# Kernel tuning notes

Hardware: AMD Instinct MI355X
Metric: run time of the kernel (lower is better)

Reference implementation:

```python
import jax, jax.numpy as jnp
import numpy as np
import math

B, S, H, NH = 2, 2048, 1024, 16
DH = H // NH  # head_dim = 64


def setup_inputs() -> dict:
    key = jax.random.key(0)
    k1, k2, k3 = jax.random.split(key, 3)
    hidden_states = jax.random.normal(k1, (B, S, H), dtype=jnp.float32)
    # causal additive mask: 0 on/below diagonal, large negative above
    causal = jnp.tril(jnp.ones((S, S), dtype=jnp.float32))
    attention_mask = jnp.where(causal == 1, 0.0, -1e9).astype(jnp.float32)
    attention_mask = jnp.broadcast_to(attention_mask[None, None], (B, 1, S, S))
    w_qkv = jax.random.normal(k2, (H, 3 * H), dtype=jnp.float32) * (H ** -0.5)
    w_out = jax.random.normal(k3, (H, H), dtype=jnp.float32) * (H ** -0.5)
    return {"hidden_states": hidden_states, "attention_mask": attention_mask,
            "w_qkv": w_qkv, "w_out": w_out}


def reference(hidden_states, attention_mask, w_qkv, w_out):
    # fused QKV projection (bias-free Linear)
    qkv = hidden_states @ w_qkv                       # [B,S,3H]
    qkv = qkv.reshape(B, S, 3, NH, DH)
    qkv = jnp.transpose(qkv, (2, 0, 3, 1, 4))         # [3,B,NH,S,DH]
    q, k, v = qkv[0], qkv[1], qkv[2]
    scores = jnp.einsum('bhqd,bhkd->bhqk', q, k) / math.sqrt(DH)
    scores = scores + attention_mask                  # [B,NH,S,S]
    probs = jax.nn.softmax(scores, axis=-1)
    ctx = jnp.einsum('bhqk,bhkd->bhqd', probs, v)     # [B,NH,S,DH]
    ctx = jnp.transpose(ctx, (0, 2, 1, 3)).reshape(B, S, H)
    return ctx @ w_out                                # [B,S,H]
```

## Files before the change

### kernel.cpp

```cpp
#include <hip/hip_runtime.h>

#define S_LEN 2048
#define NHEAD 16
#define DHEAD 64
#define HDIM  1024
#define BATCH 2
#define MTOK  (BATCH * S_LEN)

using bf16x8 = __bf16 __attribute__((ext_vector_type(8)));
using f32x4  = float __attribute__((ext_vector_type(4)));
using f32x16 = float __attribute__((ext_vector_type(16)));
using u16x4  = unsigned short __attribute__((ext_vector_type(4)));
using u32x4a = unsigned __attribute__((ext_vector_type(4)));

typedef unsigned short ushort_t;

static __device__ __forceinline__ ushort_t f2bf(float f) {
  union { float f; unsigned u; } v{f};
  unsigned r = v.u + 0x7FFFu + ((v.u >> 16) & 1u);
  return (ushort_t)(r >> 16);
}

static __device__ __forceinline__ unsigned pkbf(float a, float b) {
  return ((unsigned)f2bf(b) << 16) | (unsigned)f2bf(a);
}

static __device__ __forceinline__ unsigned cvtpk(float a, float b) {
  unsigned r;
  asm("v_cvt_pk_bf16_f32 %0, %1, %2" : "=v"(r) : "v"(a), "v"(b));
  return r;
}

static __device__ __forceinline__ bf16x8 mk8(unsigned a, unsigned b, unsigned c, unsigned d) {
  u32x4a t = {a, b, c, d};
  return __builtin_bit_cast(bf16x8, t);
}

static __device__ __forceinline__ void gload_lds16(const void* g, void* lds) {
  __builtin_amdgcn_global_load_lds(
      (const __attribute__((address_space(1))) void*)g,
      (__attribute__((address_space(3))) void*)lds, 16, 0, 0);
}

static __device__ __forceinline__ float bpermf(int paddr, float v) {
  return __builtin_bit_cast(float,
      __builtin_amdgcn_ds_bpermute(paddr, __builtin_bit_cast(int, v)));
}
static __device__ __forceinline__ unsigned bpermu(int paddr, unsigned v) {
  return (unsigned)__builtin_amdgcn_ds_bpermute(paddr, (int)v);
}

__global__ __launch_bounds__(256) void cast_bf16(const float* __restrict__ in,
                                                 ushort_t* __restrict__ out, int n4) {
  int i = blockIdx.x * blockDim.x + threadIdx.x;
  if (i >= n4) return;
  float4 v = *((const float4*)in + i);
  u16x4 o = { f2bf(v.x), f2bf(v.y), f2bf(v.z), f2bf(v.w) };
  *((u16x4*)out + i) = o;
}

__global__ void transpose_cast(const float* __restrict__ in, ushort_t* __restrict__ out,
                               int R, int C) {
  __shared__ float tile[32][33];
  int bx = blockIdx.x, by = blockIdx.y;
  int tx = threadIdx.x, ty = threadIdx.y;
  #pragma unroll
  for (int i = 0; i < 32; i += 8)
    tile[ty + i][tx] = in[(size_t)(by * 32 + ty + i) * C + bx * 32 + tx];
  __syncthreads();
  #pragma unroll
  for (int i = 0; i < 32; i += 8)
    out[(size_t)(bx * 32 + ty + i) * R + by * 32 + tx] = f2bf(tile[tx][ty + i]);
}

__global__ __launch_bounds__(512, 4) void gemm_2ph(
    const ushort_t* __restrict__ A, const ushort_t* __restrict__ Bt,
    int M, int N, int K, int mode,
    ushort_t* __restrict__ outQ, ushort_t* __restrict__ outK, ushort_t* __restrict__ outV,
    float* __restrict__ outF) {
  __shared__ __align__(16) ushort_t lA[2][128 * 32];
  __shared__ __align__(16) ushort_t lB[2][128 * 32];
  const int wg = blockIdx.x;
  const int nst = (int)(gridDim.x >> 7);
  const int xcd = wg & 7;
  const int idx = wg >> 3;
  const int stg = xcd * nst + (idx >> 4);
  const int sbm = idx & 3, sbn = (idx >> 2) & 3;
  const int bm = (stg & 7) * 4 + sbm;
  const int bn = (stg >> 3) * 4 + sbn;
  const int tid = threadIdx.x;
  const int wv = tid >> 6, lane = tid & 63;
  const int wm = wv >> 2, wn = wv & 3;
  const int lo = lane & 15, hi = lane >> 4;

  f32x4 acc[4][2] = {};

  const int srow = tid >> 2;
  const int schunk = (tid & 3) ^ ((tid >> 3) & 3);
  const ushort_t* gA = A + (size_t)(bm * 128 + srow) * K + schunk * 8;
  const ushort_t* gB = Bt + (size_t)(bn * 128 + srow) * K + schunk * 8;
  const int NT = K >> 5;

  auto stage = [&](int t) {
    const int cur = t & 1;
    char* da = (char*)&lA[cur][0] + wv * 1024 + lane * 16;
    char* db = (char*)&lB[cur][0] + wv * 1024 + lane * 16;
    gload_lds16(gA + t * 32, da);
    gload_lds16(gB + t * 32, db);
  };

  stage(0);
  for (int t = 0; t < NT; ++t) {
    const int cur = t & 1;
    if (t + 1 < NT) {
      stage(t + 1);
      asm volatile("s_waitcnt vmcnt(2)" ::: "memory");
    } else {
      asm volatile("s_waitcnt vmcnt(0)" ::: "memory");
    }
    __builtin_amdgcn_s_barrier();
    __builtin_amdgcn_sched_barrier(0);
    const ushort_t* pa = &lA[cur][0];
    const ushort_t* pb = &lB[cur][0];
    bf16x8 af[4], bfr[2];
    #pragma unroll
    for (int i = 0; i < 4; ++i) {
      int r = wm * 64 + i * 16 + lo;
      int c = hi ^ ((lo >> 1) & 3);
      af[i] = *(const bf16x8*)&pa[r * 32 + c * 8];
    }
    #pragma unroll
    for (int j = 0; j < 2; ++j) {
      int r = wn * 32 + j * 16 + lo;
      int c = hi ^ ((lo >> 1) & 3);
      bfr[j] = *(const bf16x8*)&pb[r * 32 + c * 8];
    }
    __builtin_amdgcn_s_setprio(1);
    #pragma unroll
    for (int i = 0; i < 4; ++i)
      #pragma unroll
      for (int j = 0; j < 2; ++j)
        acc[i][j] = __builtin_amdgcn_mfma_f32_16x16x32_bf16(af[i], bfr[j], acc[i][j], 0, 0, 0);
    __builtin_amdgcn_s_setprio(0);
    __builtin_amdgcn_sched_barrier(0);
    __builtin_amdgcn_s_barrier();
  }

  #pragma unroll
  for (int i = 0; i < 4; ++i) {
    #pragma unroll
    for (int j = 0; j < 2; ++j) {
      #pragma unroll
      for (int r = 0; r < 4; ++r) {
        int gm = bm * 128 + wm * 64 + i * 16 + hi * 4 + r;
        int gn = bn * 128 + wn * 32 + j * 16 + lo;
        float v = acc[i][j][r];
        if (mode == 0) {
          int which = gn >> 10;
          int h = (gn >> 6) & 15;
          int d = gn & 63;
          int b = gm >> 11;
          int s = gm & 2047;
          size_t hb = (size_t)(b * NHEAD + h) * (S_LEN * DHEAD);
          if (which == 0) {
            size_t addr = hb + (size_t)((s >> 5) * 2048 +
                          ((d >> 4) * 2 + ((d >> 3) & 1)) * 256 + (s & 31) * 8 + (d & 7));
            outQ[addr] = f2bf(v * 0.18033688011112042f);
          } else if (which == 1) {
            size_t addr = hb + (size_t)((s >> 6) * 4096 + ((s >> 5) & 1) * 2048 +
                          ((d >> 4) * 2 + ((d >> 3) & 1)) * 256 + (s & 31) * 8 + (d & 7));
            outK[addr] = f2bf(v);
          } else {
            size_t addr = hb + (size_t)((s >> 6) * 4096 + (d >> 5) * 2048 +
                          (((s >> 4) & 3) * 2 + ((s >> 3) & 1)) * 256 + (d & 31) * 8 + (s & 7));
            outV[addr] = f2bf(v);
          }
        } else {
          outF[(size_t)gm * N + gn] = v;
        }
      }
    }
  }
}

__global__ __launch_bounds__(512, 2) void attn_sw(
    const ushort_t* __restrict__ Qb, const ushort_t* __restrict__ Kb,
    const ushort_t* __restrict__ Vt, ushort_t* __restrict__ ctx) {
  const int bid = blockIdx.x;
  const int head = (bid & 7) * 4 + (bid >> 7);
  const int b16 = (bid >> 3) & 15;
  const int tid = threadIdx.x;
  const int wv = tid >> 6, lane = tid & 63;
  const int l31 = lane & 31, hi2 = lane >> 5;

  __shared__ float ldsAcc[4][32][64];
  __shared__ float ldsL[4][64];

  const int sj = (wv < 4) ? wv : ((wv & 3) ^ 2);
  const int st = (sj == 0) ? 2 * b16 : (sj == 1) ? 2 * b16 + 1
               : (sj == 2) ? 63 - 2 * b16 : 62 - 2 * b16;
  const int qbase = st * 32;
  const int qg = qbase + l31;
  const int nbb = (qbase >> 6) + 1;
  const int nh = nbb >> 1;
  const int jb0 = (wv < 4) ? 0 : nh;
  const int jb1 = (wv < 4) ? nh : nbb;
  const int paddr = (lane ^ 32) << 2;

  const size_t hbase = (size_t)head * (S_LEN * DHEAD);
  const ushort_t* vtb = Vt + hbase;

  bf16x8 qf[4];
  {
    const ushort_t* qp = Qb + hbase + st * 2048 + lane * 8;
    #pragma unroll
    for (int si = 0; si < 4; ++si) qf[si] = *(const bf16x8*)(qp + si * 512);
  }

  f32x16 accO[2] = {};
  float l = 0.f;

  auto loadK = [&](bf16x8 (&kf)[2][4], int kvb) {
    const ushort_t* kp = Kb + hbase + (size_t)(kvb >> 6) * 4096 + lane * 8;
    #pragma unroll
    for (int t = 0; t < 2; ++t)
      #pragma unroll
      for (int si = 0; si < 4; ++si)
        kf[t][si] = *(const bf16x8*)(kp + t * 2048 + si * 512);
  };

  auto body = [&](bf16x8 (&kf)[2][4], bf16x8 (&kfn)[2][4], int jb) {
    const int kvb = jb * 64;

    bf16x8 va[2][4];
    {
      const ushort_t* vp = vtb + (size_t)jb * 4096 + lane * 8;
      #pragma unroll
      for (int dt = 0; dt < 2; ++dt)
        #pragma unroll
        for (int ks = 0; ks < 4; ++ks)
          va[dt][ks] = *(const bf16x8*)(vp + dt * 2048 + ks * 512);
    }

    if (jb + 1 < jb1) loadK(kfn, kvb + 64);

    f32x16 p[2];
    #pragma unroll
    for (int t = 0; t < 2; ++t) {
      f32x16 acc = {};
      #pragma unroll
      for (int si = 0; si < 4; ++si)
        acc = __builtin_amdgcn_mfma_f32_32x32x16_bf16(kf[t][si], qf[si], acc, 0, 0, 0);
      p[t] = acc;
    }

    if (jb == nbb - 1) {
      #pragma unroll
      for (int r = 0; r < 16; ++r) {
        int kvq = kvb + ((r & 3) + 8 * (r >> 2) + 4 * hi2);
        if (kvq > qg) p[0][r] = -1e30f;
        if (kvq + 32 > qg) p[1][r] = -1e30f;
      }
    }

    #pragma unroll
    for (int t = 0; t < 2; ++t)
      #pragma unroll
      for (int r = 0; r < 16; ++r) p[t][r] = exp2f(p[t][r] - 24.0f);

    float s16[16];
    #pragma unroll
    for (int r = 0; r < 16; ++r) s16[r] = p[0][r] + p[1][r];
    float s8[8];
    #pragma unroll
    for (int r = 0; r < 8; ++r) s8[r] = s16[r] + s16[r + 8];
    float s4[4];
    #pragma unroll
    for (int r = 0; r < 4; ++r) s4[r] = s8[r] + s8[r + 4];
    float rs = (s4[0] + s4[1]) + (s4[2] + s4[3]);
    rs += bpermf(paddr, rs);
    l += rs;

    bf16x8 PB[4];
    #pragma unroll
    for (int ks = 0; ks < 4; ++ks) {
      const int t = ks >> 1, r0 = (ks & 1) * 8;
      unsigned w0 = cvtpk(p[t][r0 + 0], p[t][r0 + 1]);
      unsigned w1 = cvtpk(p[t][r0 + 2], p[t][r0 + 3]);
      unsigned w2 = cvtpk(p[t][r0 + 4], p[t][r0 + 5]);
      unsigned w3 = cvtpk(p[t][r0 + 6], p[t][r0 + 7]);
      unsigned pw0 = bpermu(paddr, w0), pw1 = bpermu(paddr, w1);
      unsigned pw2 = bpermu(paddr, w2), pw3 = bpermu(paddr, w3);
      unsigned f0 = hi2 ? pw2 : w0;
      unsigned f1 = hi2 ? pw3 : w1;
      unsigned f2 = hi2 ? w2 : pw0;
      unsigned f3 = hi2 ? w3 : pw1;
      PB[ks] = mk8(f0, f1, f2, f3);
    }

    #pragma unroll
    for (int dt = 0; dt < 2; ++dt)
      #pragma unroll
      for (int ks = 0; ks < 4; ++ks)
        accO[dt] = __builtin_amdgcn_mfma_f32_32x32x16_bf16(va[dt][ks], PB[ks], accO[dt], 0, 0, 0);
  };

  bf16x8 kfA[2][4], kfB[2][4];
  if (jb0 < jb1) {
    loadK(kfA, jb0 * 64);
    for (int jb = jb0; jb < jb1; jb += 2) {
      body(kfA, kfB, jb);
      if (jb + 1 < jb1) body(kfB, kfA, jb + 1);
    }
  }

  if (wv >= 4) {
    #pragma unroll
    for (int dt = 0; dt < 2; ++dt)
      #pragma unroll
      for (int r = 0; r < 16; ++r)
        ldsAcc[sj][dt * 16 + r][lane] = accO[dt][r];
    ldsL[sj][lane] = l;
  }
  __syncthreads();
  if (wv < 4) {
    #pragma unroll
    for (int dt = 0; dt < 2; ++dt)
      #pragma unroll
      for (int r = 0; r < 16; ++r)
        accO[dt][r] += ldsAcc[sj][dt * 16 + r][lane];
    l += ldsL[sj][lane];

    const int b = head >> 4, h = head & 15;
    const float inv = 1.0f / l;
    ushort_t* crow = ctx + ((size_t)b * S_LEN + qg) * HDIM + h * 64;
    #pragma unroll
    for (int dt = 0; dt < 2; ++dt)
      #pragma unroll
      for (int g = 0; g < 4; ++g) {
        unsigned w0 = pkbf(accO[dt][g * 4 + 0] * inv, accO[dt][g * 4 + 1] * inv);
        unsigned w1 = pkbf(accO[dt][g * 4 + 2] * inv, accO[dt][g * 4 + 3] * inv);
        unsigned long long wl = ((unsigned long long)w1 << 32) | w0;
        *(unsigned long long*)(crow + dt * 32 + g * 8 + hi2 * 4) = wl;
      }
  }
}

extern "C" void kernel_launch(void* const* d_in, const int* in_sizes, int n_in,
                              void* d_out, int out_size, void* d_ws, size_t ws_size,
                              hipStream_t stream) {
  const float* hs   = (const float*)d_in[0];
  const float* wqkv = (const float*)d_in[2];
  const float* wout = (const float*)d_in[3];
  float* out = (float*)d_out;

  char* ws = (char*)d_ws;
  ushort_t* h_bf   = (ushort_t*)(ws + 0);
  ushort_t* wqkv_t = (ushort_t*)(ws + 8388608);
  ushort_t* wout_t = (ushort_t*)(ws + 14680064);
  ushort_t* QF     = (ushort_t*)(ws + 16777216);
  ushort_t* KF     = (ushort_t*)(ws + 25165824);
  ushort_t* VF     = (ushort_t*)(ws + 33554432);
  ushort_t* ctxb   = (ushort_t*)(ws + 41943040);

  cast_bf16<<<dim3(4096), dim3(256), 0, stream>>>(hs, h_bf, MTOK * HDIM / 4);
  transpose_cast<<<dim3(96, 32), dim3(32, 8), 0, stream>>>(wqkv, wqkv_t, HDIM, 3 * HDIM);
  transpose_cast<<<dim3(32, 32), dim3(32, 8), 0, stream>>>(wout, wout_t, HDIM, HDIM);

  gemm_2ph<<<dim3(768), dim3(512), 0, stream>>>(h_bf, wqkv_t, MTOK, 3 * HDIM, HDIM, 0,
                                                QF, KF, VF, nullptr);
  attn_sw<<<dim3(512), dim3(512), 0, stream>>>(QF, KF, VF, ctxb);
  gemm_2ph<<<dim3(256), dim3(512), 0, stream>>>(ctxb, wout_t, MTOK, HDIM, HDIM, 1,
                                                nullptr, nullptr, nullptr, out);
}
```

Baseline: 118.4 us.

## Balance causal attention work evenly across waves with flattened KV-block ranges

Replaces the fixed two-waves-per-strip split with a flattened list of all 66 KV blocks across the four query strips, giving each of 8 waves an equal contiguous slice that may span strips. Partial outputs and row sums are merged through LDS atomic adds into zero-initialised buffers, and the first four waves then normalise and write the results. This targets load imbalance between waves caused by the differing halves of the causal work. In exchange it adds LDS zeroing, an extra barrier, LDS atomics and possible repeated Q loads and pipeline restarts at strip boundaries.

```diff
diff --git a/kernel.cpp b/kernel.cpp
--- a/kernel.cpp
+++ b/kernel.cpp
@@ -192,154 +192,166 @@
   const int tid = threadIdx.x;
   const int wv = tid >> 6, lane = tid & 63;
   const int l31 = lane & 31, hi2 = lane >> 5;
+  const int paddr = (lane ^ 32) << 2;
 
   __shared__ float ldsAcc[4][32][64];
   __shared__ float ldsL[4][64];
 
-  const int sj = (wv < 4) ? wv : ((wv & 3) ^ 2);
-  const int st = (sj == 0) ? 2 * b16 : (sj == 1) ? 2 * b16 + 1
-               : (sj == 2) ? 63 - 2 * b16 : 62 - 2 * b16;
-  const int qbase = st * 32;
-  const int qg = qbase + l31;
-  const int nbb = (qbase >> 6) + 1;
-  const int nh = nbb >> 1;
-  const int jb0 = (wv < 4) ? 0 : nh;
-  const int jb1 = (wv < 4) ? nh : nbb;
-  const int paddr = (lane ^ 32) << 2;
+  const int s0 = 2 * b16, s1 = 2 * b16 + 1, s2 = 63 - 2 * b16, s3 = 62 - 2 * b16;
+  const int n0 = (s0 >> 1) + 1, n1 = (s1 >> 1) + 1, n2 = (s2 >> 1) + 1;
+  const int cum1 = n0, cum2 = n0 + n1, cum3 = n0 + n1 + n2;
+
+  {
+    float* z = &ldsAcc[0][0][0];
+    for (int i = tid; i < 4 * 32 * 64; i += 512) z[i] = 0.f;
+    if (tid < 256) (&ldsL[0][0])[tid] = 0.f;
+  }
+  __syncthreads();
 
   const size_t hbase = (size_t)head * (S_LEN * DHEAD);
   const ushort_t* vtb = Vt + hbase;
 
-  bf16x8 qf[4];
-  {
-    const ushort_t* qp = Qb + hbase + st * 2048 + lane * 8;
-    #pragma unroll
-    for (int si = 0; si < 4; ++si) qf[si] = *(const bf16x8*)(qp + si * 512);
-  }
-
-  f32x16 accO[2] = {};
-  float l = 0.f;
-
-  auto loadK = [&](bf16x8 (&kf)[2][4], int kvb) {
-    const ushort_t* kp = Kb + hbase + (size_t)(kvb >> 6) * 4096 + lane * 8;
-    #pragma unroll
-    for (int t = 0; t < 2; ++t)
-      #pragma unroll
-      for (int si = 0; si < 4; ++si)
-        kf[t][si] = *(const bf16x8*)(kp + t * 2048 + si * 512);
-  };
-
-  auto body = [&](bf16x8 (&kf)[2][4], bf16x8 (&kfn)[2][4], int jb) {
-    const int kvb = jb * 64;
-
-    bf16x8 va[2][4];
+  int u = (wv * 66) >> 3;
+  const int uend = ((wv + 1) * 66) >> 3;
+
+  while (u < uend) {
+    const int k = (u >= cum1) + (u >= cum2) + (u >= cum3);
+    const int ck  = (k == 0) ? 0 : (k == 1) ? cum1 : (k == 2) ? cum2 : cum3;
+    const int ck1 = (k == 0) ? cum1 : (k == 1) ? cum2 : (k == 2) ? cum3 : 66;
+    const int stk = (k == 0) ? s0 : (k == 1) ? s1 : (k == 2) ? s2 : s3;
+    const int nb = ck1 - ck;
+    const int jbs = u - ck;
+    const int jbe = (uend - ck < nb) ? (uend - ck) : nb;
+    const int qg = stk * 32 + l31;
+
+    bf16x8 qf[4];
     {
-      const ushort_t* vp = vtb + (size_t)jb * 4096 + lane * 8;
+      const ushort_t* qp = Qb + hbase + stk * 2048 + lane * 8;
+      #pragma unroll
+      for (int si = 0; si < 4; ++si) qf[si] = *(const bf16x8*)(qp + si * 512);
+    }
+
+    f32x16 accO[2] = {};
+    float l = 0.f;
+
+    auto loadK = [&](bf16x8 (&kf)[2][4], int jb) {
+      const ushort_t* kp = Kb + hbase + (size_t)jb * 4096 + lane * 8;
+      #pragma unroll
+      for (int t = 0; t < 2; ++t)
+        #pragma unroll
+        for (int si = 0; si < 4; ++si)
+          kf[t][si] = *(const bf16x8*)(kp + t * 2048 + si * 512);
+    };
+
+    auto body = [&](bf16x8 (&kf)[2][4], bf16x8 (&kfn)[2][4], int jb) {
+      bf16x8 va[2][4];
+      {
+        const ushort_t* vp = vtb + (size_t)jb * 4096 + lane * 8;
+        #pragma unroll
+        for (int dt = 0; dt < 2; ++dt)
+          #pragma unroll
+          for (int ks = 0; ks < 4; ++ks)
+            va[dt][ks] = *(const bf16x8*)(vp + dt * 2048 + ks * 512);
+      }
+
+      if (jb + 1 < jbe) loadK(kfn, jb + 1);
+
+      f32x16 p[2];
+      #pragma unroll
+      for (int t = 0; t < 2; ++t) {
+        f32x16 acc = {};
+        #pragma unroll
+        for (int si = 0; si < 4; ++si)
+          acc = __builtin_amdgcn_mfma_f32_32x32x16_bf16(kf[t][si], qf[si], acc, 0, 0, 0);
+        p[t] = acc;
+      }
+
+      if (jb == nb - 1) {
+        #pragma unroll
+        for (int r = 0; r < 16; ++r) {
+          int kvq = jb * 64 + ((r & 3) + 8 * (r >> 2) + 4 * hi2);
+          if (kvq > qg) p[0][r] = -1e30f;
+          if (kvq + 32 > qg) p[1][r] = -1e30f;
+        }
+      }
+
+      #pragma unroll
+      for (int t = 0; t < 2; ++t)
+        #pragma unroll
+        for (int r = 0; r < 16; ++r) p[t][r] = exp2f(p[t][r] - 24.0f);
+
+      float s16[16];
+      #pragma unroll
+      for (int r = 0; r < 16; ++r) s16[r] = p[0][r] + p[1][r];
+      float s8[8];
+      #pragma unroll
+      for (int r = 0; r < 8; ++r) s8[r] = s16[r] + s16[r + 8];
+      float s4[4];
+      #pragma unroll
+      for (int r = 0; r < 4; ++r) s4[r] = s8[r] + s8[r + 4];
+      float rs = (s4[0] + s4[1]) + (s4[2] + s4[3]);
+      rs += bpermf(paddr, rs);
+      l += rs;
+
+      bf16x8 PB[4];
+      #pragma unroll
+      for (int ks = 0; ks < 4; ++ks) {
+        const int t = ks >> 1, r0 = (ks & 1) * 8;
+        unsigned w0 = cvtpk(p[t][r0 + 0], p[t][r0 + 1]);
+        unsigned w1 = cvtpk(p[t][r0 + 2], p[t][r0 + 3]);
+        unsigned w2 = cvtpk(p[t][r0 + 4], p[t][r0 + 5]);
+        unsigned w3 = cvtpk(p[t][r0 + 6], p[t][r0 + 7]);
+        unsigned pw0 = bpermu(paddr, w0), pw1 = bpermu(paddr, w1);
+        unsigned pw2 = bpermu(paddr, w2), pw3 = bpermu(paddr, w3);
+        unsigned f0 = hi2 ? pw2 : w0;
+        unsigned f1 = hi2 ? pw3 : w1;
+        unsigned f2 = hi2 ? w2 : pw0;
+        unsigned f3 = hi2 ? w3 : pw1;
+        PB[ks] = mk8(f0, f1, f2, f3);
+      }
+
       #pragma unroll
       for (int dt = 0; dt < 2; ++dt)
         #pragma unroll
         for (int ks = 0; ks < 4; ++ks)
-          va[dt][ks] = *(const bf16x8*)(vp + dt * 2048 + ks * 512);
-    }
-
-    if (jb + 1 < jb1) loadK(kfn, kvb + 64);
-
-    f32x16 p[2];
-    #pragma unroll
-    for (int t = 0; t < 2; ++t) {
-      f32x16 acc = {};
-      #pragma unroll
-      for (int si = 0; si < 4; ++si)
-        acc = __builtin_amdgcn_mfma_f32_32x32x16_bf16(kf[t][si], qf[si], acc, 0, 0, 0);
-      p[t] = acc;
-    }
-
-    if (jb == nbb - 1) {
-      #pragma unroll
-      for (int r = 0; r < 16; ++r) {
-        int kvq = kvb + ((r & 3) + 8 * (r >> 2) + 4 * hi2);
-        if (kvq > qg) p[0][r] = -1e30f;
-        if (kvq + 32 > qg) p[1][r] = -1e30f;
-      }
-    }
-
-    #pragma unroll
-    for (int t = 0; t < 2; ++t)
-      #pragma unroll
-      for (int r = 0; r < 16; ++r) p[t][r] = exp2f(p[t][r] - 24.0f);
-
-    float s16[16];
-    #pragma unroll
-    for (int r = 0; r < 16; ++r) s16[r] = p[0][r] + p[1][r];
-    float s8[8];
-    #pragma unroll
-    for (int r = 0; r < 8; ++r) s8[r] = s16[r] + s16[r + 8];
-    float s4[4];
-    #pragma unroll
-    for (int r = 0; r < 4; ++r) s4[r] = s8[r] + s8[r + 4];
-    float rs = (s4[0] + s4[1]) + (s4[2] + s4[3]);
-    rs += bpermf(paddr, rs);
-    l += rs;
-
-    bf16x8 PB[4];
-    #pragma unroll
-    for (int ks = 0; ks < 4; ++ks) {
-      const int t = ks >> 1, r0 = (ks & 1) * 8;
-      unsigned w0 = cvtpk(p[t][r0 + 0], p[t][r0 + 1]);
-      unsigned w1 = cvtpk(p[t][r0 + 2], p[t][r0 + 3]);
-      unsigned w2 = cvtpk(p[t][r0 + 4], p[t][r0 + 5]);
-      unsigned w3 = cvtpk(p[t][r0 + 6], p[t][r0 + 7]);
-      unsigned pw0 = bpermu(paddr, w0), pw1 = bpermu(paddr, w1);
-      unsigned pw2 = bpermu(paddr, w2), pw3 = bpermu(paddr, w3);
-      unsigned f0 = hi2 ? pw2 : w0;
-      unsigned f1 = hi2 ? pw3 : w1;
-      unsigned f2 = hi2 ? w2 : pw0;
-      unsigned f3 = hi2 ? w3 : pw1;
-      PB[ks] = mk8(f0, f1, f2, f3);
+          accO[dt] = __builtin_amdgcn_mfma_f32_32x32x16_bf16(va[dt][ks], PB[ks], accO[dt], 0, 0, 0);
+    };
+
+    bf16x8 kfA[2][4], kfB[2][4];
+    loadK(kfA, jbs);
+    for (int jb = jbs; jb < jbe; jb += 2) {
+      body(kfA, kfB, jb);
+      if (jb + 1 < jbe) body(kfB, kfA, jb + 1);
     }
 
     #pragma unroll
     for (int dt = 0; dt < 2; ++dt)
       #pragma unroll
-      for (int ks = 0; ks < 4; ++ks)
-        accO[dt] = __builtin_amdgcn_mfma_f32_32x32x16_bf16(va[dt][ks], PB[ks], accO[dt], 0, 0, 0);
-  };
-
-  bf16x8 kfA[2][4], kfB[2][4];
-  if (jb0 < jb1) {
-    loadK(kfA, jb0 * 64);
-    for (int jb = jb0; jb < jb1; jb += 2) {
-      body(kfA, kfB, jb);
-      if (jb + 1 < jb1) body(kfB, kfA, jb + 1);
-    }
-  }
-
-  if (wv >= 4) {
-    #pragma unroll
-    for (int dt = 0; dt < 2; ++dt)
-      #pragma unroll
       for (int r = 0; r < 16; ++r)
-        ldsAcc[sj][dt * 16 + r][lane] = accO[dt][r];
-    ldsL[sj][lane] = l;
-  }
+        atomicAdd(&ldsAcc[k][dt * 16 + r][lane], accO[dt][r]);
+    atomicAdd(&ldsL[k][lane], l);
+
+    u = ck + jbe;
+  }
+
   __syncthreads();
   if (wv < 4) {
+    const int k = wv;
+    const int stk = (k == 0) ? s0 : (k == 1) ? s1 : (k == 2) ? s2 : s3;
+    const int qg = stk * 32 + l31;
+    const float inv = 1.0f / ldsL[k][lane];
+    const int b = head >> 4, h = head & 15;
+    ushort_t* crow = ctx + ((size_t)b * S_LEN + qg) * HDIM + h * 64;
     #pragma unroll
     for (int dt = 0; dt < 2; ++dt)
       #pragma unroll
-      for (int r = 0; r < 16; ++r)
-        accO[dt][r] += ldsAcc[sj][dt * 16 + r][lane];
-    l += ldsL[sj][lane];
-
-    const int b = head >> 4, h = head & 15;
-    const float inv = 1.0f / l;
-    ushort_t* crow = ctx + ((size_t)b * S_LEN + qg) * HDIM + h * 64;
-    #pragma unroll
-    for (int dt = 0; dt < 2; ++dt)
-      #pragma unroll
       for (int g = 0; g < 4; ++g) {
-        unsigned w0 = pkbf(accO[dt][g * 4 + 0] * inv, accO[dt][g * 4 + 1] * inv);
-        unsigned w1 = pkbf(accO[dt][g * 4 + 2] * inv, accO[dt][g * 4 + 3] * inv);
+        float v0 = ldsAcc[k][dt * 16 + g * 4 + 0][lane] * inv;
+        float v1 = ldsAcc[k][dt * 16 + g * 4 + 1][lane] * inv;
+        float v2 = ldsAcc[k][dt * 16 + g * 4 + 2][lane] * inv;
+        float v3 = ldsAcc[k][dt * 16 + g * 4 + 3][lane] * inv;
+        unsigned w0 = pkbf(v0, v1);
+        unsigned w1 = pkbf(v2, v3);
         unsigned long long wl = ((unsigned long long)w1 << 32) | w0;
         *(unsigned long long*)(crow + dt * 32 + g * 8 + hi2 * 4) = wl;
       }
```

Result: slower. 164.2 us (+38.6%).
